# Kernel tuning notes

Measured on AMD Instinct MI355X. Metric: run time of the kernel, lower is better.

Reference implementation:

```python
import jax, jax.numpy as jnp
import numpy as np

NUM_HEADS = 16
EMB_SIZE = 1024
HEAD_SIZE = 64


def setup_inputs() -> dict:
    key = jax.random.key(0)
    ks = jax.random.split(key, 9)
    H, E, D = NUM_HEADS, EMB_SIZE, HEAD_SIZE
    s = 1.0 / np.sqrt(E)
    X = jax.random.normal(ks[0], (4, 2048, E), dtype=jnp.float32)
    Wq = jax.random.uniform(ks[1], (H, E, D), jnp.float32, -s, s)
    Wk = jax.random.uniform(ks[2], (H, E, D), jnp.float32, -s, s)
    Wv = jax.random.uniform(ks[3], (H, E, D), jnp.float32, -s, s)
    bq = jax.random.uniform(ks[4], (H, D), jnp.float32, -s, s)
    bk = jax.random.uniform(ks[5], (H, D), jnp.float32, -s, s)
    bv = jax.random.uniform(ks[6], (H, D), jnp.float32, -s, s)
    so = 1.0 / np.sqrt(H * D)
    Wo = jax.random.uniform(ks[7], (H * D, E), jnp.float32, -so, so)
    bo = jax.random.uniform(ks[8], (E,), jnp.float32, -so, so)
    return {"X": X, "Wq": Wq, "Wk": Wk, "Wv": Wv, "bq": bq, "bk": bk, "bv": bv, "Wo": Wo, "bo": bo}


def reference(X, Wq, Wk, Wv, bq, bk, bv, Wo, bo):
    B, S, E = X.shape
    H, _, D = Wq.shape
    # per-head projections (batched over heads)
    q = jnp.einsum('bse,hed->bhsd', X, Wq) + bq[None, :, None, :]
    k = jnp.einsum('bse,hed->bhsd', X, Wk) + bk[None, :, None, :]
    v = jnp.einsum('bse,hed->bhsd', X, Wv) + bv[None, :, None, :]
    # causal scaled-dot-product attention
    scores = jnp.einsum('bhsd,bhtd->bhst', q, k) / jnp.sqrt(jnp.float32(D))
    causal = jnp.tril(jnp.ones((S, S), dtype=bool))
    scores = jnp.where(causal[None, None], scores, jnp.float32(-jnp.inf))
    probs = jax.nn.softmax(scores, axis=-1)
    out = jnp.einsum('bhst,bhtd->bhsd', probs, v)
    # concat heads (head h occupies slots [h*D:(h+1)*D]) then output proj
    concat = out.transpose(0, 2, 1, 3).reshape(B, S, H * D)
    # dropout is identity in eval mode
    return concat @ Wo + bo
```

## Files before the change

kernel.cpp:

```cpp
#include <hip/hip_runtime.h>
#include <stdint.h>


typedef float   f32x4  __attribute__((ext_vector_type(4)));
typedef __bf16  bf16x8 __attribute__((ext_vector_type(8)));
typedef short   short8 __attribute__((ext_vector_type(8)));
typedef unsigned short ushort4v __attribute__((ext_vector_type(4)));

typedef __attribute__((address_space(1))) void GV;
typedef __attribute__((address_space(3))) void LV;

#define DEVI static __device__ __forceinline__

DEVI unsigned short f2bf(float f){
  unsigned u = __float_as_uint(f);
  unsigned r = u + 0x7fffu + ((u>>16)&1u);
  return (unsigned short)(r>>16);
}

DEVI unsigned cvt_pk_bf16(float lo, float hi){
  unsigned r;
  asm("v_cvt_pk_bf16_f32 %0, %1, %2" : "=v"(r) : "v"(lo), "v"(hi));
  return r;
}

DEVI void permlane32_swap(unsigned &a, unsigned &b){
  asm volatile("v_permlane32_swap_b32 %0, %1" : "+v"(a), "+v"(b));
}
DEVI void permlane16_swap(unsigned &a, unsigned &b){
  asm volatile("v_permlane16_swap_b32 %0, %1" : "+v"(a), "+v"(b));
}

DEVI void gl_lds16(const void* g, void* l){
  __builtin_amdgcn_global_load_lds((GV*)g, (LV*)l, 16, 0, 0);
}

__global__ __launch_bounds__(256) void pack_x(const float* __restrict__ X,
                                              short* __restrict__ Xb){
  int i = blockIdx.x*256 + threadIdx.x;
  const float4* p = (const float4*)(X + (size_t)i*8);
  float4 a = p[0], b = p[1];
  short8 o;
  o[0]=(short)f2bf(a.x); o[1]=(short)f2bf(a.y); o[2]=(short)f2bf(a.z); o[3]=(short)f2bf(a.w);
  o[4]=(short)f2bf(b.x); o[5]=(short)f2bf(b.y); o[6]=(short)f2bf(b.z); o[7]=(short)f2bf(b.w);
  *(short8*)(Xb + (size_t)i*8) = o;
}

__global__ __launch_bounds__(256) void pack_wqkv(const float* __restrict__ Wq,
                                                 const float* __restrict__ Wk,
                                                 const float* __restrict__ Wv,
                                                 short* __restrict__ Wp){
  int t = blockIdx.x*256 + threadIdx.x;
  int n = t >> 7, kc = t & 127;
  int which = n >> 10, hd = n & 1023, h = hd >> 6, d = hd & 63;
  const float* W = which==0 ? Wq : (which==1 ? Wk : Wv);
  const float* src = W + ((size_t)h*1024 + kc*8)*64 + d;
  short8 o;
  #pragma unroll
  for (int j=0;j<8;++j) o[j] = (short)f2bf(src[(size_t)j*64]);
  *(short8*)(Wp + (size_t)n*1024 + kc*8) = o;
}

__global__ __launch_bounds__(256) void pack_wo(const float* __restrict__ Wo,
                                               short* __restrict__ WoT){
  int t = blockIdx.x*256 + threadIdx.x;
  int n = t >> 7, kc = t & 127;
  const float* src = Wo + (size_t)(kc*8)*1024 + n;
  short8 o;
  #pragma unroll
  for (int j=0;j<8;++j) o[j] = (short)f2bf(src[(size_t)j*1024]);
  *(short8*)(WoT + (size_t)n*1024 + kc*8) = o;
}

template<int MODE>
__global__ __launch_bounds__(512)
void gemm256(const short* __restrict__ A, const short* __restrict__ Bt,
             const float* __restrict__ b0, const float* __restrict__ b1,
             const float* __restrict__ b2,
             short* __restrict__ Qb, short* __restrict__ Kb, short* __restrict__ Vtb,
             float* __restrict__ Out)
{
  __shared__ __align__(16) char sm[3][49152];
  const int K2 = 2048;
  int t = threadIdx.x, lane = t & 63, wid = t >> 6;
  int wr = wid >> 2, wc = wid & 3;
  int l15 = lane & 15, l4 = lane >> 4;
  int nwg = gridDim.x, qd = nwg >> 3;
  int swz = (blockIdx.x & 7) * qd + (blockIdx.x >> 3);
  int bm = swz & 63, bn = swz >> 6;
  size_t abase = (size_t)bm * 128 * K2;
  size_t bbase = (size_t)bn * 256 * K2;

  f32x4 acc[4][4] = {};

  auto stage = [&](int kt, char* buf){
    int kb = kt * 128;
    #pragma unroll
    for (int c = 0; c < 2; ++c){
      int x = c*8192 + t*16;
      int r = x >> 7, z = x & 127;
      int zs = z ^ ((r & 7) << 4);
      gl_lds16((const char*)A + abase + (size_t)r*K2 + kb + zs, buf + c*8192 + wid*1024);
    }
    #pragma unroll
    for (int c = 0; c < 4; ++c){
      int x = c*8192 + t*16;
      int r = x >> 7, z = x & 127;
      int zs = z ^ ((r & 7) << 4);
      gl_lds16((const char*)Bt + bbase + (size_t)r*K2 + kb + zs, buf + 16384 + c*8192 + wid*1024);
    }
  };

  auto compute = [&](const char* buf){
    const char* sA = buf;
    const char* sB = buf + 16384;
    #pragma unroll
    for (int kk = 0; kk < 2; ++kk){
      bf16x8 af[4], bfr[4];
      int cb = kk*64 + l4*16;
      #pragma unroll
      for (int i = 0; i < 4; ++i){
        int ra = wr*64 + i*16 + l15;
        af[i]  = *(const bf16x8*)(sA + ra*128 + (cb ^ ((ra&7)<<4)));
        int rb = wc*64 + i*16 + l15;
        bfr[i] = *(const bf16x8*)(sB + rb*128 + (cb ^ ((rb&7)<<4)));
      }
      __builtin_amdgcn_s_setprio(1);
      #pragma unroll
      for (int i = 0; i < 4; ++i)
        #pragma unroll
        for (int j = 0; j < 4; ++j)
          acc[i][j] = __builtin_amdgcn_mfma_f32_16x16x32_bf16(af[i], bfr[j], acc[i][j], 0, 0, 0);
      __builtin_amdgcn_s_setprio(0);
    }
  };

  stage(0, sm[0]);
  stage(1, sm[1]);
  for (int kt = 0; kt < 14; ++kt){
    stage(kt + 2, sm[(kt + 2) % 3]);
    asm volatile("s_waitcnt vmcnt(12)\n\ts_barrier" ::: "memory");
    compute(sm[kt % 3]);
    asm volatile("s_barrier" ::: "memory");
  }
  asm volatile("s_waitcnt vmcnt(6)\n\ts_barrier" ::: "memory");
  compute(sm[2]);
  asm volatile("s_waitcnt vmcnt(0)" ::: "memory");
  compute(sm[0]);

  #pragma unroll
  for (int i = 0; i < 4; ++i){
    int mbase = bm*128 + wr*64 + i*16 + l4*4;
    #pragma unroll
    for (int j = 0; j < 4; ++j){
      int n = bn*256 + wc*64 + j*16 + l15;
      if (MODE == 0){
        int which = n >> 10, hd = n & 1023, h = hd >> 6, d = hd & 63;
        const float* bp = which==0 ? b0 : (which==1 ? b1 : b2);
        float bias = bp[hd];
        int b = mbase >> 11, sbase = mbase & 2047;
        size_t bh = (size_t)(b*16 + h);
        if (which == 2){
          ushort4v pv;
          #pragma unroll
          for (int r = 0; r < 4; ++r) pv[r] = f2bf(acc[i][j][r] + bias);
          *(ushort4v*)(Vtb + (bh*64 + d)*2048 + sbase) = pv;
        } else {
          short* dst = (which==0 ? Qb : Kb) + bh*2048*64;
          float sc = which==0 ? 0.18033688f : 1.0f;
          #pragma unroll
          for (int r = 0; r < 4; ++r)
            dst[(size_t)(sbase + r)*64 + d] = (short)f2bf((acc[i][j][r] + bias) * sc);
        }
      } else {
        float bias = b0[n];
        #pragma unroll
        for (int r = 0; r < 4; ++r)
          Out[(size_t)(mbase + r)*1024 + n] = acc[i][j][r] + bias;
      }
    }
  }
}

__global__ __launch_bounds__(256, 5)
void attn(const short* __restrict__ Qb, const short* __restrict__ Kb,
          const short* __restrict__ Vtb, short* __restrict__ Ob)
{
  __shared__ __align__(16) char smK[2][8192];
  __shared__ __align__(16) char smV[2][8192];
  int t = threadIdx.x, lane = t & 63, wid = t >> 6;
  int l15 = lane & 15, hi = lane >> 4;
  int hi16 = hi*16, hi4 = hi*4;
  int bh = blockIdx.x & 63;
  int qb = 31 - (blockIdx.x >> 6);
  int b = bh >> 4, h = bh & 15;
  int wq0 = qb*64 + wid*16;
  const char* Qh = (const char*)(Qb + (size_t)bh*2048*64);
  const char* Kh = (const char*)(Kb + (size_t)bh*2048*64);
  const char* Vh = (const char*)(Vtb + (size_t)bh*64*2048);

  bf16x8 vones;
  #pragma unroll
  for (int z = 0; z < 8; ++z) vones[z] = (__bf16)1.0f;

  bf16x8 qf[2];
  #pragma unroll
  for (int kk = 0; kk < 2; ++kk)
    qf[kk] = *(const bf16x8*)(Qh + (size_t)(wq0 + l15)*128 + kk*64 + hi16);

  f32x4 oacc[4] = {};
  f32x4 lacc = {};
  float m = -1e30f;

  int nkt = qb + 1;

  #pragma unroll
  for (int c = 0; c < 2; ++c){
    int x = c*4096 + t*16;
    int r = x >> 7, z = x & 127;
    int zs = z ^ ((r & 7) << 4);
    gl_lds16(Kh + (size_t)r*128 + zs, smK[0] + c*4096 + wid*1024);
    gl_lds16(Vh + (size_t)r*4096 + zs, smV[0] + c*4096 + wid*1024);
  }
  __syncthreads();

  for (int kt = 0; kt < nkt; ++kt){
    int cur = kt & 1;
    if (kt + 1 < nkt){
      int nxt = cur ^ 1;
      #pragma unroll
      for (int c = 0; c < 2; ++c){
        int x = c*4096 + t*16;
        int r = x >> 7, z = x & 127;
        int zs = z ^ ((r & 7) << 4);
        gl_lds16(Kh + (size_t)(kt+1)*8192 + (size_t)r*128 + zs, smK[nxt] + c*4096 + wid*1024);
        gl_lds16(Vh + (size_t)r*4096 + (size_t)(kt+1)*128 + zs, smV[nxt] + c*4096 + wid*1024);
      }
    }
    const char* Kc = smK[cur];
    const char* Vc = smV[cur];
    int kbase = kt * 64;

    f32x4 sa[4];
    __builtin_amdgcn_s_setprio(1);
    #pragma unroll
    for (int nt = 0; nt < 4; ++nt){
      f32x4 a = {};
      #pragma unroll
      for (int kk = 0; kk < 2; ++kk){
        int rk = nt*16 + l15;
        bf16x8 kf = *(const bf16x8*)(Kc + rk*128 + ((kk*64 + hi16) ^ ((rk&7)<<4)));
        a = __builtin_amdgcn_mfma_f32_16x16x32_bf16(kf, qf[kk], a, 0, 0, 0);
      }
      sa[nt] = a;
    }
    __builtin_amdgcn_s_setprio(0);

    if (kt == qb){
      int qrow = wq0 + l15;
      #pragma unroll
      for (int nt = 0; nt < 4; ++nt)
        #pragma unroll
        for (int r = 0; r < 4; ++r)
          if (kbase + nt*16 + hi4 + r > qrow) sa[nt][r] = -1e30f;
    }

    float pm;
    {
      float t0 = fmaxf(fmaxf(sa[0][0], sa[0][1]), sa[0][2]);
      float t1 = fmaxf(fmaxf(sa[0][3], sa[1][0]), sa[1][1]);
      float t2 = fmaxf(fmaxf(sa[1][2], sa[1][3]), sa[2][0]);
      float t3 = fmaxf(fmaxf(sa[2][1], sa[2][2]), sa[2][3]);
      float t4 = fmaxf(fmaxf(sa[3][0], sa[3][1]), sa[3][2]);
      float u0 = fmaxf(fmaxf(t0, t1), sa[3][3]);
      float u1 = fmaxf(fmaxf(t2, t3), t4);
      pm = fmaxf(u0, u1);
    }
    pm = fmaxf(pm, __shfl_xor(pm, 16));
    pm = fmaxf(pm, __shfl_xor(pm, 32));
    if (!__all(pm <= m + 8.0f)){
      float mnew = fmaxf(m, pm);
      float sc = exp2f(m - mnew);
      lacc *= sc;
      #pragma unroll
      for (int dt = 0; dt < 4; ++dt) oacc[dt] *= sc;
      m = mnew;
    }
    unsigned pw[8];
    #pragma unroll
    for (int nt = 0; nt < 4; ++nt){
      float p0 = exp2f(sa[nt][0] - m);
      float p1 = exp2f(sa[nt][1] - m);
      float p2 = exp2f(sa[nt][2] - m);
      float p3 = exp2f(sa[nt][3] - m);
      pw[nt*2]   = cvt_pk_bf16(p0, p1);
      pw[nt*2+1] = cvt_pk_bf16(p2, p3);
    }

    union U { unsigned u[4]; bf16x8 v; } f0, f1;
    {
      unsigned a0 = pw[0], b0v = pw[2];
      permlane32_swap(a0, b0v); permlane16_swap(a0, b0v);
      unsigned a1 = pw[1], b1v = pw[3];
      permlane32_swap(a1, b1v); permlane16_swap(a1, b1v);
      f0.u[0] = a0; f0.u[1] = a1; f0.u[2] = b0v; f0.u[3] = b1v;
      unsigned a2 = pw[4], b2v = pw[6];
      permlane32_swap(a2, b2v); permlane16_swap(a2, b2v);
      unsigned a3 = pw[5], b3v = pw[7];
      permlane32_swap(a3, b3v); permlane16_swap(a3, b3v);
      f1.u[0] = a2; f1.u[1] = a3; f1.u[2] = b2v; f1.u[3] = b3v;
    }

    __builtin_amdgcn_s_setprio(1);
    #pragma unroll
    for (int kk = 0; kk < 2; ++kk){
      bf16x8 pf = kk ? f1.v : f0.v;
      lacc = __builtin_amdgcn_mfma_f32_16x16x32_bf16(vones, pf, lacc, 0, 0, 0);
      #pragma unroll
      for (int dt = 0; dt < 4; ++dt){
        int rv = dt*16 + l15;
        bf16x8 vf = *(const bf16x8*)(Vc + rv*128 + ((kk*64 + hi16) ^ ((rv&7)<<4)));
        oacc[dt] = __builtin_amdgcn_mfma_f32_16x16x32_bf16(vf, pf, oacc[dt], 0, 0, 0);
      }
    }
    __builtin_amdgcn_s_setprio(0);

    __syncthreads();
  }

  float inv = 1.0f / lacc[0];
  int srow = wq0 + l15;
  size_t rb = ((size_t)(b*2048 + srow))*1024 + h*64 + hi4;
  #pragma unroll
  for (int dt = 0; dt < 4; ++dt){
    unsigned w0 = cvt_pk_bf16(oacc[dt][0]*inv, oacc[dt][1]*inv);
    unsigned w1 = cvt_pk_bf16(oacc[dt][2]*inv, oacc[dt][3]*inv);
    *(unsigned long long*)(Ob + rb + dt*16) =
        ((unsigned long long)w1 << 32) | (unsigned long long)w0;
  }
}

extern "C" void kernel_launch(void* const* d_in, const int* in_sizes, int n_in,
                              void* d_out, int out_size, void* d_ws, size_t ws_size,
                              hipStream_t stream)
{
  const float* X  = (const float*)d_in[0];
  const float* Wq = (const float*)d_in[1];
  const float* Wk = (const float*)d_in[2];
  const float* Wv = (const float*)d_in[3];
  const float* bq = (const float*)d_in[4];
  const float* bk = (const float*)d_in[5];
  const float* bv = (const float*)d_in[6];
  const float* Wo = (const float*)d_in[7];
  const float* bo = (const float*)d_in[8];
  float* Out = (float*)d_out;

  char* ws = (char*)d_ws;
  short* Xbf  = (short*)(ws);
  short* Wp   = (short*)(ws + 16777216);
  short* WoT  = (short*)(ws + 23068672);
  short* Qb   = (short*)(ws + 25165824);
  short* Kb   = (short*)(ws + 41943040);
  short* Vtb  = (short*)(ws + 58720256);
  short* Ob   = (short*)(ws + 75497472);

  pack_x   <<<4096, 256, 0, stream>>>(X, Xbf);
  pack_wqkv<<<1536, 256, 0, stream>>>(Wq, Wk, Wv, Wp);
  pack_wo  <<< 512, 256, 0, stream>>>(Wo, WoT);

  gemm256<0><<<768, 512, 0, stream>>>(Xbf, Wp, bq, bk, bv, Qb, Kb, Vtb, nullptr);
  attn      <<<2048, 256, 0, stream>>>(Qb, Kb, Vtb, Ob);
  gemm256<1><<<256, 512, 0, stream>>>(Ob, WoT, bo, nullptr, nullptr,
                                      nullptr, nullptr, nullptr, Out);
}
```

Before: 196.7 us.

## Interleave GEMM global-to-LDS staging with MFMA sub-phases and barriers

Restructures the 256-wide GEMM main loop so that the next stage's global-to-LDS loads are split into three chunks (A, B first half, B second half) and issued between finer-grained LDS reads and MFMA groups, with barriers separating each phase. This aims to spread memory issue across the compute and keep MFMA units busy while loads are in flight, in the style of a ping-pong schedule. It adds many more s_barrier instructions per iteration, which can add synchronisation overhead if waves do not need to be aligned.

```diff
diff --git a/kernel.cpp b/kernel.cpp
--- a/kernel.cpp
+++ b/kernel.cpp
@@ -34,6 +34,8 @@
 DEVI void gl_lds16(const void* g, void* l){
   __builtin_amdgcn_global_load_lds((GV*)g, (LV*)l, 16, 0, 0);
 }
+
+#define BAR() asm volatile("s_barrier" ::: "memory")
 
 __global__ __launch_bounds__(256) void pack_x(const float* __restrict__ X,
                                               short* __restrict__ Xb){
@@ -92,8 +94,10 @@
   size_t bbase = (size_t)bn * 256 * K2;
 
   f32x4 acc[4][4] = {};
-
-  auto stage = [&](int kt, char* buf){
+  const char* sA; const char* sB;
+  bf16x8 af[4], bfr[4];
+
+  auto stageA = [&](int kt, char* buf){
     int kb = kt * 128;
     #pragma unroll
     for (int c = 0; c < 2; ++c){
@@ -102,51 +106,66 @@
       int zs = z ^ ((r & 7) << 4);
       gl_lds16((const char*)A + abase + (size_t)r*K2 + kb + zs, buf + c*8192 + wid*1024);
     }
-    #pragma unroll
-    for (int c = 0; c < 4; ++c){
-      int x = c*8192 + t*16;
+  };
+  auto stageB = [&](int kt, char* buf, int c0){
+    int kb = kt * 128;
+    #pragma unroll
+    for (int c = 0; c < 2; ++c){
+      int cc = c0 + c;
+      int x = cc*8192 + t*16;
       int r = x >> 7, z = x & 127;
       int zs = z ^ ((r & 7) << 4);
-      gl_lds16((const char*)Bt + bbase + (size_t)r*K2 + kb + zs, buf + 16384 + c*8192 + wid*1024);
-    }
-  };
-
-  auto compute = [&](const char* buf){
-    const char* sA = buf;
-    const char* sB = buf + 16384;
-    #pragma unroll
-    for (int kk = 0; kk < 2; ++kk){
-      bf16x8 af[4], bfr[4];
-      int cb = kk*64 + l4*16;
-      #pragma unroll
-      for (int i = 0; i < 4; ++i){
-        int ra = wr*64 + i*16 + l15;
-        af[i]  = *(const bf16x8*)(sA + ra*128 + (cb ^ ((ra&7)<<4)));
-        int rb = wc*64 + i*16 + l15;
-        bfr[i] = *(const bf16x8*)(sB + rb*128 + (cb ^ ((rb&7)<<4)));
-      }
-      __builtin_amdgcn_s_setprio(1);
-      #pragma unroll
-      for (int i = 0; i < 4; ++i)
-        #pragma unroll
-        for (int j = 0; j < 4; ++j)
-          acc[i][j] = __builtin_amdgcn_mfma_f32_16x16x32_bf16(af[i], bfr[j], acc[i][j], 0, 0, 0);
-      __builtin_amdgcn_s_setprio(0);
-    }
-  };
-
-  stage(0, sm[0]);
-  stage(1, sm[1]);
-  for (int kt = 0; kt < 14; ++kt){
-    stage(kt + 2, sm[(kt + 2) % 3]);
-    asm volatile("s_waitcnt vmcnt(12)\n\ts_barrier" ::: "memory");
-    compute(sm[kt % 3]);
-    asm volatile("s_barrier" ::: "memory");
-  }
-  asm volatile("s_waitcnt vmcnt(6)\n\ts_barrier" ::: "memory");
-  compute(sm[2]);
-  asm volatile("s_waitcnt vmcnt(0)" ::: "memory");
-  compute(sm[0]);
+      gl_lds16((const char*)Bt + bbase + (size_t)r*K2 + kb + zs, buf + 16384 + cc*8192 + wid*1024);
+    }
+  };
+  auto rd_af = [&](int kk){
+    int cb = kk*64 + l4*16;
+    #pragma unroll
+    for (int i = 0; i < 4; ++i){
+      int ra = wr*64 + i*16 + l15;
+      af[i] = *(const bf16x8*)(sA + ra*128 + (cb ^ ((ra&7)<<4)));
+    }
+  };
+  auto rd_bf = [&](int kk, int j0){
+    int cb = kk*64 + l4*16;
+    #pragma unroll
+    for (int j = 0; j < 2; ++j){
+      int rb = wc*64 + (j0 + j)*16 + l15;
+      bfr[j0 + j] = *(const bf16x8*)(sB + rb*128 + (cb ^ ((rb&7)<<4)));
+    }
+  };
+  auto mm = [&](int j0){
+    __builtin_amdgcn_s_setprio(1);
+    #pragma unroll
+    for (int i = 0; i < 4; ++i)
+      #pragma unroll
+      for (int j = 0; j < 2; ++j)
+        acc[i][j0+j] = __builtin_amdgcn_mfma_f32_16x16x32_bf16(af[i], bfr[j0+j], acc[i][j0+j], 0, 0, 0);
+    __builtin_amdgcn_s_setprio(0);
+  };
+
+  stageA(0, sm[0]); stageB(0, sm[0], 0); stageB(0, sm[0], 2);
+  stageA(1, sm[1]); stageB(1, sm[1], 0); stageB(1, sm[1], 2);
+
+  for (int kt = 0; kt < 16; ++kt){
+    if (kt == 15) asm volatile("s_waitcnt vmcnt(0)" ::: "memory");
+    else          asm volatile("s_waitcnt vmcnt(6)" ::: "memory");
+    BAR();
+    sA = sm[kt % 3]; sB = sA + 16384;
+    char* nb = sm[(kt + 2) % 3];
+    bool st = kt < 14;
+    rd_af(0); rd_bf(0, 0);
+    if (st) stageA(kt + 2, nb);
+    BAR(); mm(0); BAR();
+    rd_bf(0, 2);
+    if (st) stageB(kt + 2, nb, 0);
+    BAR(); mm(2); BAR();
+    rd_af(1); rd_bf(1, 0);
+    if (st) stageB(kt + 2, nb, 2);
+    BAR(); mm(0); BAR();
+    rd_bf(1, 2);
+    BAR(); mm(2);
+  }
 
   #pragma unroll
   for (int i = 0; i < 4; ++i){
```

After: 194.4 us. About the same (-1.2%).
